# Optimization experiments

Measured on AMD Instinct MI355X. Metric: run time of the kernel, lower is better.

## Reference

```python
import jax, jax.numpy as jnp
import numpy as np

B, N, C, H = 8, 4096, 512, 8
HD = C // H  # head_dim = 64
SCALE = HD ** -0.5


def setup_inputs() -> dict:
    key = jax.random.key(0)
    k1, k2, k3, k4 = jax.random.split(key, 4)
    x1 = jax.random.normal(k1, (B, N, C), dtype=jnp.float32)
    x2 = jax.random.normal(k2, (B, N, C), dtype=jnp.float32)
    # nn.Linear(dim, 2*dim, bias=False) weights; stored as [in, out] for x @ W
    lim = 1.0 / np.sqrt(C)
    W_kv1 = jax.random.uniform(k3, (C, 2 * C), dtype=jnp.float32, minval=-lim, maxval=lim)
    W_kv2 = jax.random.uniform(k4, (C, 2 * C), dtype=jnp.float32, minval=-lim, maxval=lim)
    return {"x1": x1, "x2": x2, "W_kv1": W_kv1, "W_kv2": W_kv2}


def _heads(t):
    # [B, N, C] -> [B, H, N, HD]
    return t.reshape(B, N, H, HD).transpose(0, 2, 1, 3)


def _kv(x, W):
    kv = (x @ W).reshape(B, N, 2, H, HD)  # [B, N, 2, H, HD]
    kv = kv.transpose(2, 0, 3, 1, 4)      # [2, B, H, N, HD]
    return kv[0], kv[1]


def _ctx(k, v):
    # K^T V: [B, H, HD, HD], scaled then softmax over axis -2 (the k-feature axis)
    ctx = jnp.einsum("bhnd,bhne->bhde", k, v) * SCALE
    return jax.nn.softmax(ctx, axis=-2)


def reference(x1, x2, W_kv1, W_kv2):
    q1 = _heads(x1)
    q2 = _heads(x2)
    k1, v1 = _kv(x1, W_kv1)
    k2, v2 = _kv(x2, W_kv2)
    ctx1 = _ctx(k1, v1)
    ctx2 = _ctx(k2, v2)
    # cross: q1 attends via ctx2, q2 via ctx1
    o1 = jnp.einsum("bhnd,bhde->bhne", q1, ctx2).transpose(0, 2, 1, 3).reshape(B, N, C)
    o2 = jnp.einsum("bhnd,bhde->bhne", q2, ctx1).transpose(0, 2, 1, 3).reshape(B, N, C)
    return o1, o2
```

## Files before the change

kernel.cpp:

```cpp
#include <hip/hip_runtime.h>
#include <stdint.h>
#include <stddef.h>

#define NB 8
#define NSEQ 4096
#define NC 512
#define NH 8
#define SWZ(c) ((((c) >> 2) ^ (c)) & 7)

typedef __attribute__((ext_vector_type(4))) float f4;
typedef __attribute__((ext_vector_type(8))) short bf8;
typedef __attribute__((ext_vector_type(4))) short bf4;
typedef __attribute__((ext_vector_type(2))) unsigned int u32x2;
typedef __attribute__((ext_vector_type(4))) unsigned int u32x4;

__device__ __forceinline__ short f2bf(float f) {
  union { float f; unsigned int u; } v; v.f = f;
  unsigned int u = v.u + 0x7FFFu + ((v.u >> 16) & 1u);
  return (short)(u >> 16);
}
__device__ __forceinline__ float bf2f(short h) {
  union { unsigned int u; float f; } v;
  v.u = ((unsigned int)(unsigned short)h) << 16;
  return v.f;
}
__device__ __forceinline__ unsigned int cvtpk(float a, float b) {
  unsigned int r;
  asm("v_cvt_pk_bf16_f32 %0, %1, %2" : "=v"(r) : "v"(a), "v"(b));
  return r;
}

__global__ __launch_bounds__(256) void k_wt(const float* __restrict__ W0,
                                            const float* __restrict__ W1,
                                            short* __restrict__ Wth,
                                            short* __restrict__ Wtl) {
  __shared__ float t[64 * 65];
  int bid = blockIdx.x;
  int ot = bid & 15;
  int ct = (bid >> 4) & 7;
  int s = bid >> 7;
  const float* W = s ? W1 : W0;
  const float* src = W + (size_t)(ct * 64) * 1024 + ot * 64;
  int tid = threadIdx.x;
  int rr = tid >> 4, c4 = (tid & 15) * 4;
#pragma unroll
  for (int p = 0; p < 4; ++p) {
    int c = p * 16 + rr;
    f4 v = *(const f4*)&src[(size_t)c * 1024 + c4];
#pragma unroll
    for (int i = 0; i < 4; ++i) t[(c4 + i) * 65 + c] = v[i];
  }
  __syncthreads();
  size_t obase = (size_t)s * 524288 + (size_t)(ot * 64) * 512 + ct * 64;
#pragma unroll
  for (int p = 0; p < 4; ++p) {
    int o = p * 16 + rr;
    bf4 vh, vl;
#pragma unroll
    for (int i = 0; i < 4; ++i) {
      float v = t[o * 65 + c4 + i];
      short h = f2bf(v);
      vh[i] = h; vl[i] = f2bf(v - bf2f(h));
    }
    *(bf4*)&Wth[obase + (size_t)o * 512 + c4] = vh;
    *(bf4*)&Wtl[obase + (size_t)o * 512 + c4] = vl;
  }
}

__global__ __launch_bounds__(256) void k_xbt(const float* __restrict__ x0,
                                             const float* __restrict__ x1,
                                             short* __restrict__ XbT) {
  __shared__ short t[64 * 64];
  int bx = blockIdx.x;
  int ct = bx & 7;
  int nt = (bx >> 3) & 63;
  int b  = (bx >> 9) & 7;
  int s  = bx >> 12;
  const float* x = s ? x1 : x0;
  const float* xb = x + ((size_t)b * NSEQ + (size_t)nt * 64) * NC + ct * 64;
  int tid = threadIdx.x;
  int c4 = (tid & 15) * 4;
  int nb = (tid >> 4) * 4;
  int g = nb >> 3;
  int nlo = nb & 7;
  f4 v[4];
#pragma unroll
  for (int i = 0; i < 4; ++i)
    v[i] = *(const f4*)&xb[(size_t)(nb + i) * NC + c4];
#pragma unroll
  for (int ci = 0; ci < 4; ++ci) {
    int c = c4 + ci;
    int soff = c * 64 + ((g ^ SWZ(c)) << 3) + nlo;
    u32x2 wa;
    wa[0] = cvtpk(v[0][ci], v[1][ci]);
    wa[1] = cvtpk(v[2][ci], v[3][ci]);
    *(u32x2*)&t[soff] = wa;
  }
  __syncthreads();
  int gg = tid & 7;
  int cr = tid >> 3;
  short* Xp = XbT + ((size_t)(s * 8 + b) * NC + (size_t)ct * 64) * NSEQ + (size_t)nt * 64;
#pragma unroll
  for (int p = 0; p < 2; ++p) {
    int c = cr + p * 32;
    bf8 vv = *(const bf8*)&t[c * 64 + ((gg ^ SWZ(c)) << 3)];
    *(bf8*)&Xp[(size_t)c * NSEQ + gg * 8] = vv;
  }
}

__global__ __launch_bounds__(256) void k_gram(const short* __restrict__ XbT,
                                              float* __restrict__ G32) {
  __shared__ short Ab[3][64 * 64];
  __shared__ short Bb[3][64 * 64];
  int bid = blockIdx.x;
  int xcd = bid & 7;
  int j = bid >> 3;
  int sb = xcd + ((j >= 36) ? 8 : 0);
  int p = (j >= 36) ? (j - 36) : j;
  int ti = 0;
  while (p >= 8 - ti) { p -= 8 - ti; ++ti; }
  int tj = ti + p;
  int diag = (ti == tj);
  const short* Ar = XbT + ((size_t)sb * NC + ti * 64) * NSEQ;
  const short* Br = XbT + ((size_t)sb * NC + tj * 64) * NSEQ;
  int tid = threadIdx.x;
  int lane = tid & 63;
  int w = tid >> 6;
  int lrow = lane >> 3;
  int lgr = lane & 7;
  int wr = w & 1, wc = w >> 1;
  int mrow = lane & 15;
  int kreg = lane >> 4;
  f4 z = {0.f, 0.f, 0.f, 0.f};
  f4 acc[2][2];
#pragma unroll
  for (int i = 0; i < 2; ++i)
#pragma unroll
    for (int jq = 0; jq < 2; ++jq) acc[i][jq] = z;

  auto stage = [&](int t) {
    int buf = t % 3;
    int k0 = t * 64;
#pragma unroll
    for (int q = 0; q < 2; ++q) {
      int r0 = q * 32 + w * 8;
      int arow = r0 + lrow;
      int gsw = (lgr ^ lrow) << 3;
      __builtin_amdgcn_global_load_lds(
          (const unsigned int*)(Ar + (size_t)arow * NSEQ + k0 + gsw),
          (unsigned int*)&Ab[buf][r0 * 64], 16, 0, 0);
      if (!diag)
        __builtin_amdgcn_global_load_lds(
            (const unsigned int*)(Br + (size_t)arow * NSEQ + k0 + gsw),
            (unsigned int*)&Bb[buf][r0 * 64], 16, 0, 0);
    }
  };
  auto comp = [&](int buf) {
    const short* Abuf = Ab[buf];
    const short* Bbuf = diag ? Ab[buf] : Bb[buf];
#pragma unroll
    for (int kk = 0; kk < 2; ++kk) {
      int gr = kk * 4 + kreg;
      bf8 a[2], bb[2];
#pragma unroll
      for (int i = 0; i < 2; ++i) {
        int ra = wr * 32 + i * 16 + mrow;
        a[i] = *(const bf8*)&Abuf[ra * 64 + ((gr ^ (ra & 7)) << 3)];
        int rb2 = wc * 32 + i * 16 + mrow;
        bb[i] = *(const bf8*)&Bbuf[rb2 * 64 + ((gr ^ (rb2 & 7)) << 3)];
      }
#pragma unroll
      for (int i = 0; i < 2; ++i)
#pragma unroll
        for (int jq = 0; jq < 2; ++jq)
          acc[i][jq] = __builtin_amdgcn_mfma_f32_16x16x32_bf16(a[i], bb[jq], acc[i][jq], 0, 0, 0);
    }
  };

  stage(0);
  stage(1);
  for (int t = 0; t < 64; ++t) {
    if (t < 63) {
      if (diag) { asm volatile("s_waitcnt vmcnt(2)" ::: "memory"); }
      else      { asm volatile("s_waitcnt vmcnt(4)" ::: "memory"); }
    } else {
      asm volatile("s_waitcnt vmcnt(0)" ::: "memory");
    }
    __builtin_amdgcn_sched_barrier(0);
    __builtin_amdgcn_s_barrier();
    __builtin_amdgcn_sched_barrier(0);
    if (t + 2 < 64) stage(t + 2);
    __builtin_amdgcn_sched_barrier(0);
    comp(t % 3);
  }

  float* Gp = G32 + (size_t)sb * NC * NC;
  int rb = ti * 64 + wr * 32 + (lane >> 4) * 4;
  int cb = tj * 64 + wc * 32 + (lane & 15);
#pragma unroll
  for (int i = 0; i < 2; ++i)
#pragma unroll
    for (int jq = 0; jq < 2; ++jq)
#pragma unroll
      for (int r = 0; r < 4; ++r)
        Gp[(size_t)(rb + i * 16 + r) * NC + cb + jq * 16] = acc[i][jq][r];
}

__global__ __launch_bounds__(256) void k_sym(const float* __restrict__ G32,
                                             short* __restrict__ Gh,
                                             short* __restrict__ Gl) {
  __shared__ float t[64 * 65];
  int bid = blockIdx.x;
  int tile = bid & 63;
  int sb = bid >> 6;
  int ti = tile >> 3, tj = tile & 7;
  int tr = ti > tj;
  const float* src = G32 + (size_t)sb * 262144
                   + (tr ? ((size_t)(tj * 64) * 512 + ti * 64)
                         : ((size_t)(ti * 64) * 512 + tj * 64));
  int tid = threadIdx.x;
  int rr = tid >> 4;
  int c4 = (tid & 15) * 4;
#pragma unroll
  for (int p = 0; p < 4; ++p) {
    int r = p * 16 + rr;
    f4 v = *(const f4*)&src[(size_t)r * 512 + c4];
    if (tr) {
#pragma unroll
      for (int i = 0; i < 4; ++i) t[(c4 + i) * 65 + r] = v[i];
    } else {
#pragma unroll
      for (int i = 0; i < 4; ++i) t[r * 65 + c4 + i] = v[i];
    }
  }
  __syncthreads();
  size_t obase = (size_t)sb * 262144 + (size_t)(ti * 64) * 512 + tj * 64;
#pragma unroll
  for (int p = 0; p < 4; ++p) {
    int r = p * 16 + rr;
    bf4 vh, vl;
#pragma unroll
    for (int i = 0; i < 4; ++i) {
      float v = t[r * 65 + c4 + i] * 0.125f;
      short h = f2bf(v);
      vh[i] = h; vl[i] = f2bf(v - bf2f(h));
    }
    *(bf4*)&Gh[obase + (size_t)r * 512 + c4] = vh;
    *(bf4*)&Gl[obase + (size_t)r * 512 + c4] = vl;
  }
}

__global__ __launch_bounds__(256) void k_t(const short* __restrict__ Wth,
                                           const short* __restrict__ Wtl,
                                           const short* __restrict__ Gh,
                                           const short* __restrict__ Gl,
                                           float* __restrict__ Ttf) {
  __shared__ short Ah[128 * 40];
  __shared__ short Al[128 * 40];
  __shared__ short Bh[128 * 40];
  __shared__ short Bl[128 * 40];
  int tid = threadIdx.x;
  int et = blockIdx.x & 3;
  int ct = blockIdx.x >> 2;
  int sb = blockIdx.y;
  int s = sb >> 3;
  const short* Avh = Wth + ((size_t)s * 1024 + 512 + (size_t)et * 128) * NC;
  const short* Avl = Wtl + ((size_t)s * 1024 + 512 + (size_t)et * 128) * NC;
  const short* Gph = Gh + (size_t)sb * 262144 + (size_t)(ct * 128) * 512;
  const short* Gpl = Gl + (size_t)sb * 262144 + (size_t)(ct * 128) * 512;
  int cc = tid >> 1;
  int kh = (tid & 1) * 16;
  int lane = tid & 63;
  int w = tid >> 6;
  int wm = (w & 1) * 64;
  int wn = (w >> 1) * 64;
  int mrow = lane & 15;
  int kcol = (lane >> 4) * 8;
  f4 z = {0.f, 0.f, 0.f, 0.f};
  f4 acc[4][4];
#pragma unroll
  for (int i = 0; i < 4; ++i)
#pragma unroll
    for (int j = 0; j < 4; ++j) acc[i][j] = z;

  for (int it = 0; it < 16; ++it) {
    int k0 = it * 32;
    __syncthreads();
    *(bf8*)&Ah[cc * 40 + kh]     = *(const bf8*)&Avh[(size_t)cc * NC + k0 + kh];
    *(bf8*)&Ah[cc * 40 + kh + 8] = *(const bf8*)&Avh[(size_t)cc * NC + k0 + kh + 8];
    *(bf8*)&Al[cc * 40 + kh]     = *(const bf8*)&Avl[(size_t)cc * NC + k0 + kh];
    *(bf8*)&Al[cc * 40 + kh + 8] = *(const bf8*)&Avl[(size_t)cc * NC + k0 + kh + 8];
    *(bf8*)&Bh[cc * 40 + kh]     = *(const bf8*)&Gph[(size_t)cc * 512 + k0 + kh];
    *(bf8*)&Bh[cc * 40 + kh + 8] = *(const bf8*)&Gph[(size_t)cc * 512 + k0 + kh + 8];
    *(bf8*)&Bl[cc * 40 + kh]     = *(const bf8*)&Gpl[(size_t)cc * 512 + k0 + kh];
    *(bf8*)&Bl[cc * 40 + kh + 8] = *(const bf8*)&Gpl[(size_t)cc * 512 + k0 + kh + 8];
    __syncthreads();
    bf8 ah[4], al[4], bh[4], bl[4];
#pragma unroll
    for (int i = 0; i < 4; ++i) {
      ah[i] = *(const bf8*)&Ah[(wm + i * 16 + mrow) * 40 + kcol];
      al[i] = *(const bf8*)&Al[(wm + i * 16 + mrow) * 40 + kcol];
      bh[i] = *(const bf8*)&Bh[(wn + i * 16 + mrow) * 40 + kcol];
      bl[i] = *(const bf8*)&Bl[(wn + i * 16 + mrow) * 40 + kcol];
    }
#pragma unroll
    for (int i = 0; i < 4; ++i)
#pragma unroll
      for (int j = 0; j < 4; ++j) {
        acc[i][j] = __builtin_amdgcn_mfma_f32_16x16x32_bf16(ah[i], bh[j], acc[i][j], 0, 0, 0);
        acc[i][j] = __builtin_amdgcn_mfma_f32_16x16x32_bf16(ah[i], bl[j], acc[i][j], 0, 0, 0);
        acc[i][j] = __builtin_amdgcn_mfma_f32_16x16x32_bf16(al[i], bh[j], acc[i][j], 0, 0, 0);
      }
  }
  float* Tp = Ttf + (size_t)sb * NC * NC;
  int rb = et * 128 + wm + (lane >> 4) * 4;
  int cb = ct * 128 + wn + (lane & 15);
#pragma unroll
  for (int i = 0; i < 4; ++i)
#pragma unroll
    for (int j = 0; j < 4; ++j)
#pragma unroll
      for (int r = 0; r < 4; ++r)
        Tp[(size_t)(rb + i * 16 + r) * NC + cb + j * 16] = acc[i][j][r];
}

__global__ __launch_bounds__(256) void k_ctx(const short* __restrict__ Wth,
                                             const short* __restrict__ Wtl,
                                             const float* __restrict__ Ttf,
                                             short* __restrict__ ctxT) {
  __shared__ short Ah[64 * 72];
  __shared__ short Al[64 * 72];
  __shared__ short Bh[64 * 72];
  __shared__ short Bl[64 * 72];
  __shared__ float Sf[64 * 68];
  int tid = threadIdx.x;
  int h = blockIdx.x & 7;
  int sb = blockIdx.x >> 3;
  int s = sb >> 3;
  const short* Akh = Wth + ((size_t)s * 1024 + (size_t)h * 64) * NC;
  const short* Akl = Wtl + ((size_t)s * 1024 + (size_t)h * 64) * NC;
  const float* Bt = Ttf + ((size_t)sb * NC + (size_t)h * 64) * NC;
  int cs = tid >> 3;
  int kg = (tid & 7) * 8;
  int lane = tid & 63;
  int w = tid >> 6;
  int mrow = lane & 15;
  int kcol = (lane >> 4) * 8;
  f4 z = {0.f, 0.f, 0.f, 0.f};
  f4 acc[4];
#pragma unroll
  for (int j = 0; j < 4; ++j) acc[j] = z;

  for (int it = 0; it < 8; ++it) {
    int k0 = it * 64;
    __syncthreads();
#pragma unroll
    for (int r = 0; r < 2; ++r) {
      int d = cs + r * 32;
      *(bf8*)&Ah[d * 72 + kg] = *(const bf8*)&Akh[(size_t)d * NC + k0 + kg];
      *(bf8*)&Al[d * 72 + kg] = *(const bf8*)&Akl[(size_t)d * NC + k0 + kg];
      f4 g0 = *(const f4*)&Bt[(size_t)d * NC + k0 + kg];
      f4 g1 = *(const f4*)&Bt[(size_t)d * NC + k0 + kg + 4];
      bf8 vh, vl;
#pragma unroll
      for (int i = 0; i < 4; ++i) {
        short hh = f2bf(g0[i]);
        vh[i] = hh; vl[i] = f2bf(g0[i] - bf2f(hh));
        hh = f2bf(g1[i]);
        vh[i + 4] = hh; vl[i + 4] = f2bf(g1[i] - bf2f(hh));
      }
      *(bf8*)&Bh[d * 72 + kg] = vh;
      *(bf8*)&Bl[d * 72 + kg] = vl;
    }
    __syncthreads();
#pragma unroll
    for (int kk = 0; kk < 2; ++kk) {
      bf8 ah = *(const bf8*)&Ah[(w * 16 + mrow) * 72 + kk * 32 + kcol];
      bf8 al = *(const bf8*)&Al[(w * 16 + mrow) * 72 + kk * 32 + kcol];
#pragma unroll
      for (int j = 0; j < 4; ++j) {
        bf8 bh = *(const bf8*)&Bh[(j * 16 + mrow) * 72 + kk * 32 + kcol];
        bf8 bl = *(const bf8*)&Bl[(j * 16 + mrow) * 72 + kk * 32 + kcol];
        acc[j] = __builtin_amdgcn_mfma_f32_16x16x32_bf16(ah, bh, acc[j], 0, 0, 0);
        acc[j] = __builtin_amdgcn_mfma_f32_16x16x32_bf16(ah, bl, acc[j], 0, 0, 0);
        acc[j] = __builtin_amdgcn_mfma_f32_16x16x32_bf16(al, bh, acc[j], 0, 0, 0);
      }
    }
  }
  __syncthreads();
#pragma unroll
  for (int j = 0; j < 4; ++j)
#pragma unroll
    for (int r = 0; r < 4; ++r)
      Sf[(w * 16 + (lane >> 4) * 4 + r) * 68 + j * 16 + (lane & 15)] = acc[j][r];
  __syncthreads();
  if (tid < 64) {
    int e = tid;
    float mx = -1e30f;
    for (int d = 0; d < 64; ++d) mx = fmaxf(mx, Sf[d * 68 + e]);
    float sum = 0.f;
    for (int d = 0; d < 64; ++d) {
      float ev = __expf(Sf[d * 68 + e] - mx);
      sum += ev;
      Sf[d * 68 + e] = ev;
    }
    float rs = 1.f / sum;
    short* cp = ctxT + (((size_t)sb * NH + h) * 64 + e) * 64;
    for (int d0 = 0; d0 < 64; d0 += 4) {
      bf4 ov;
      ov[0] = f2bf(Sf[(d0 + 0) * 68 + e] * rs);
      ov[1] = f2bf(Sf[(d0 + 1) * 68 + e] * rs);
      ov[2] = f2bf(Sf[(d0 + 2) * 68 + e] * rs);
      ov[3] = f2bf(Sf[(d0 + 3) * 68 + e] * rs);
      *(bf4*)&cp[d0] = ov;
    }
  }
}

__global__ __launch_bounds__(256) void k_o(const float* __restrict__ x0,
                                           const float* __restrict__ x1,
                                           const short* __restrict__ ctxT,
                                           float* __restrict__ out) {
  __shared__ short Ab[128 * 72];
  __shared__ short Bb[64 * 72];
  int tid = threadIdx.x;
  int bx = blockIdx.x;
  int nt = bx & 31;
  int h = (bx >> 5) & 7;
  int b = (bx >> 8) & 7;
  int so = bx >> 11;
  const float* x = so ? x1 : x0;
  const short* cp = ctxT + (((size_t)(1 - so) * NB + b) * NH + h) * 64 * 64;
  {
    int e = tid >> 2;
    int dg = (tid & 3) * 16;
    *(bf8*)&Bb[e * 72 + dg] = *(const bf8*)&cp[e * 64 + dg];
    *(bf8*)&Bb[e * 72 + dg + 8] = *(const bf8*)&cp[e * 64 + dg + 8];
  }
  const float* xp = x + ((size_t)b * NSEQ + (size_t)nt * 128) * NC + h * 64;
  {
    int n = tid >> 1;
    int dh = (tid & 1) * 32;
    const float* row = xp + (size_t)n * NC + dh;
#pragma unroll
    for (int q = 0; q < 4; ++q) {
      f4 v0 = *(const f4*)&row[q * 8];
      f4 v1 = *(const f4*)&row[q * 8 + 4];
      u32x4 pw;
      pw[0] = cvtpk(v0[0], v0[1]);
      pw[1] = cvtpk(v0[2], v0[3]);
      pw[2] = cvtpk(v1[0], v1[1]);
      pw[3] = cvtpk(v1[2], v1[3]);
      *(u32x4*)&Ab[n * 72 + dh + q * 8] = pw;
    }
  }
  __syncthreads();
  int lane = tid & 63;
  int w = tid >> 6;
  int mrow = lane & 15;
  int kcol = (lane >> 4) * 8;
  f4 z = {0.f, 0.f, 0.f, 0.f};
  f4 acc[2][4];
#pragma unroll
  for (int i = 0; i < 2; ++i)
#pragma unroll
    for (int j = 0; j < 4; ++j) acc[i][j] = z;
#pragma unroll
  for (int kk = 0; kk < 2; ++kk) {
    bf8 a0 = *(const bf8*)&Ab[(w * 32 + mrow) * 72 + kk * 32 + kcol];
    bf8 a1 = *(const bf8*)&Ab[(w * 32 + 16 + mrow) * 72 + kk * 32 + kcol];
#pragma unroll
    for (int j = 0; j < 4; ++j) {
      bf8 bv = *(const bf8*)&Bb[(j * 16 + mrow) * 72 + kk * 32 + kcol];
      acc[0][j] = __builtin_amdgcn_mfma_f32_16x16x32_bf16(a0, bv, acc[0][j], 0, 0, 0);
      acc[1][j] = __builtin_amdgcn_mfma_f32_16x16x32_bf16(a1, bv, acc[1][j], 0, 0, 0);
    }
  }
  float* op = out + (size_t)so * ((size_t)NB * NSEQ * NC)
            + ((size_t)b * NSEQ + (size_t)nt * 128) * NC + h * 64;
#pragma unroll
  for (int i = 0; i < 2; ++i)
#pragma unroll
    for (int j = 0; j < 4; ++j)
#pragma unroll
      for (int r = 0; r < 4; ++r)
        op[(size_t)(w * 32 + i * 16 + (lane >> 4) * 4 + r) * NC + j * 16 + (lane & 15)] = acc[i][j][r];
}

extern "C" void kernel_launch(void* const* d_in, const int* in_sizes, int n_in,
                              void* d_out, int out_size, void* d_ws, size_t ws_size,
                              hipStream_t stream) {
  const float* x1 = (const float*)d_in[0];
  const float* x2 = (const float*)d_in[1];
  const float* W1 = (const float*)d_in[2];
  const float* W2 = (const float*)d_in[3];
  float* out = (float*)d_out;
  char* ws = (char*)d_ws;
  short* XbT  = (short*)ws;
  float* Ttf  = (float*)ws;
  short* Gh   = (short*)(ws + 16777216);
  short* Gl   = (short*)(ws + 25165824);
  short* Wth  = (short*)(ws + 67108864);
  short* Wtl  = (short*)(ws + 69206016);
  float* G32  = (float*)(ws + 71303168);
  short* ctxT = (short*)(ws + 88080384);

  hipLaunchKernelGGL(k_wt,   dim3(256),    dim3(256), 0, stream, W1, W2, Wth, Wtl);
  hipLaunchKernelGGL(k_xbt,  dim3(8192),   dim3(256), 0, stream, x1, x2, XbT);
  hipLaunchKernelGGL(k_gram, dim3(576),    dim3(256), 0, stream, XbT, G32);
  hipLaunchKernelGGL(k_sym,  dim3(1024),   dim3(256), 0, stream, G32, Gh, Gl);
  hipLaunchKernelGGL(k_t,    dim3(16, 16), dim3(256), 0, stream, Wth, Wtl, Gh, Gl, Ttf);
  hipLaunchKernelGGL(k_ctx,  dim3(128),    dim3(256), 0, stream, Wth, Wtl, Ttf, ctxT);
  hipLaunchKernelGGL(k_o,    dim3(4096),   dim3(256), 0, stream, x1, x2, ctxT, out);
}
```

Measured before the change: 184.2 us.

## Split off-diagonal Gram tiles along K, sum halves in k_sym, stage k_o output

The Gram kernel now uses 1024 blocks instead of 576. Off-diagonal tiles are split into two K halves: one half writes to the upper triangle, the other to the transposed lower slot. This balances work, since diagonal tiles run 64 iterations and each off-diagonal half runs 32. k_sym sums the upper and lower partials for off-diagonal tiles. The pipeline drops from triple buffering with manual vmcnt waits to double buffering with __syncthreads, which may expose more load latency. k_o now stages its output through LDS so rows are written to global memory with contiguous f4 stores.

```diff
diff --git a/kernel.cpp b/kernel.cpp
--- a/kernel.cpp
+++ b/kernel.cpp
@@ -110,19 +110,23 @@
 
 __global__ __launch_bounds__(256) void k_gram(const short* __restrict__ XbT,
                                               float* __restrict__ G32) {
-  __shared__ short Ab[3][64 * 64];
-  __shared__ short Bb[3][64 * 64];
+  __shared__ short Ab[2][64 * 64];
+  __shared__ short Bb[2][64 * 64];
   int bid = blockIdx.x;
-  int xcd = bid & 7;
-  int j = bid >> 3;
-  int sb = xcd + ((j >= 36) ? 8 : 0);
-  int p = (j >= 36) ? (j - 36) : j;
+  int L = (bid & 7) * 128 + (bid >> 3);
+  int sb = L >> 6;
+  int v = L & 63;
+  int half = (v >= 36);
+  int p = half ? v - 36 : v;
   int ti = 0;
-  while (p >= 8 - ti) { p -= 8 - ti; ++ti; }
-  int tj = ti + p;
-  int diag = (ti == tj);
-  const short* Ar = XbT + ((size_t)sb * NC + ti * 64) * NSEQ;
-  const short* Br = XbT + ((size_t)sb * NC + tj * 64) * NSEQ;
+  if (!half) { while (p >= 8 - ti) { p -= 8 - ti; ++ti; } }
+  else       { while (p >= 7 - ti) { p -= 7 - ti; ++ti; } }
+  int tj = half ? (ti + 1 + p) : (ti + p);
+  int diag = (!half) && (ti == tj);
+  int NIT = diag ? 64 : 32;
+  int kbase = half ? 2048 : 0;
+  const short* Ar = XbT + ((size_t)sb * NC + ti * 64) * NSEQ + kbase;
+  const short* Br = XbT + ((size_t)sb * NC + tj * 64) * NSEQ + kbase;
   int tid = threadIdx.x;
   int lane = tid & 63;
   int w = tid >> 6;
@@ -138,9 +142,7 @@
 #pragma unroll
     for (int jq = 0; jq < 2; ++jq) acc[i][jq] = z;
 
-  auto stage = [&](int t) {
-    int buf = t % 3;
-    int k0 = t * 64;
+  auto stage = [&](int buf, int k0) {
 #pragma unroll
     for (int q = 0; q < 2; ++q) {
       int r0 = q * 32 + w * 8;
@@ -177,26 +179,18 @@
     }
   };
 
-  stage(0);
-  stage(1);
-  for (int t = 0; t < 64; ++t) {
-    if (t < 63) {
-      if (diag) { asm volatile("s_waitcnt vmcnt(2)" ::: "memory"); }
-      else      { asm volatile("s_waitcnt vmcnt(4)" ::: "memory"); }
-    } else {
-      asm volatile("s_waitcnt vmcnt(0)" ::: "memory");
-    }
-    __builtin_amdgcn_sched_barrier(0);
-    __builtin_amdgcn_s_barrier();
-    __builtin_amdgcn_sched_barrier(0);
-    if (t + 2 < 64) stage(t + 2);
-    __builtin_amdgcn_sched_barrier(0);
-    comp(t % 3);
+  stage(0, 0);
+  for (int t = 0; t < NIT; ++t) {
+    __syncthreads();
+    if (t + 1 < NIT) stage((t + 1) & 1, (t + 1) * 64);
+    comp(t & 1);
   }
 
   float* Gp = G32 + (size_t)sb * NC * NC;
-  int rb = ti * 64 + wr * 32 + (lane >> 4) * 4;
-  int cb = tj * 64 + wc * 32 + (lane & 15);
+  int rpart = wr * 32 + (lane >> 4) * 4;
+  int cpart = wc * 32 + (lane & 15);
+  int rb = (half ? tj : ti) * 64 + rpart;
+  int cb = (half ? ti : tj) * 64 + cpart;
 #pragma unroll
   for (int i = 0; i < 2; ++i)
 #pragma unroll
@@ -215,22 +209,27 @@
   int sb = bid >> 6;
   int ti = tile >> 3, tj = tile & 7;
   int tr = ti > tj;
-  const float* src = G32 + (size_t)sb * 262144
-                   + (tr ? ((size_t)(tj * 64) * 512 + ti * 64)
-                         : ((size_t)(ti * 64) * 512 + tj * 64));
+  int umin = tr ? tj : ti, umax = tr ? ti : tj;
+  int offd = (umin != umax);
+  const float* srcU = G32 + (size_t)sb * 262144 + (size_t)(umin * 64) * 512 + umax * 64;
+  const float* srcL = G32 + (size_t)sb * 262144 + (size_t)(umax * 64) * 512 + umin * 64;
   int tid = threadIdx.x;
   int rr = tid >> 4;
   int c4 = (tid & 15) * 4;
 #pragma unroll
   for (int p = 0; p < 4; ++p) {
     int r = p * 16 + rr;
-    f4 v = *(const f4*)&src[(size_t)r * 512 + c4];
+    f4 vv = *(const f4*)&srcU[(size_t)r * 512 + c4];
+    if (offd) {
+      f4 v2 = *(const f4*)&srcL[(size_t)r * 512 + c4];
+      vv += v2;
+    }
     if (tr) {
 #pragma unroll
-      for (int i = 0; i < 4; ++i) t[(c4 + i) * 65 + r] = v[i];
+      for (int i = 0; i < 4; ++i) t[(c4 + i) * 65 + r] = vv[i];
     } else {
 #pragma unroll
-      for (int i = 0; i < 4; ++i) t[r * 65 + c4 + i] = v[i];
+      for (int i = 0; i < 4; ++i) t[r * 65 + c4 + i] = vv[i];
     }
   }
   __syncthreads();
@@ -421,8 +420,10 @@
                                            const float* __restrict__ x1,
                                            const short* __restrict__ ctxT,
                                            float* __restrict__ out) {
-  __shared__ short Ab[128 * 72];
-  __shared__ short Bb[64 * 72];
+  __shared__ float U[8704];
+  short* Ab = (short*)U;
+  short* Bb = (short*)U + 128 * 72;
+  float* OutT = U;
   int tid = threadIdx.x;
   int bx = blockIdx.x;
   int nt = bx & 31;
@@ -476,15 +477,22 @@
       acc[1][j] = __builtin_amdgcn_mfma_f32_16x16x32_bf16(a1, bv, acc[1][j], 0, 0, 0);
     }
   }
-  float* op = out + (size_t)so * ((size_t)NB * NSEQ * NC)
-            + ((size_t)b * NSEQ + (size_t)nt * 128) * NC + h * 64;
+  __syncthreads();
 #pragma unroll
   for (int i = 0; i < 2; ++i)
 #pragma unroll
     for (int j = 0; j < 4; ++j)
 #pragma unroll
       for (int r = 0; r < 4; ++r)
-        op[(size_t)(w * 32 + i * 16 + (lane >> 4) * 4 + r) * NC + j * 16 + (lane & 15)] = acc[i][j][r];
+        OutT[(w * 32 + i * 16 + (lane >> 4) * 4 + r) * 68 + j * 16 + (lane & 15)] = acc[i][j][r];
+  __syncthreads();
+  int r2 = tid >> 1;
+  int ch = (tid & 1) * 32;
+  float* op2 = out + (size_t)so * ((size_t)NB * NSEQ * NC)
+             + ((size_t)b * NSEQ + (size_t)nt * 128 + r2) * NC + h * 64 + ch;
+#pragma unroll
+  for (int q = 0; q < 8; ++q)
+    *(f4*)&op2[q * 4] = *(const f4*)&OutT[r2 * 68 + ch + q * 4];
 }
 
 extern "C" void kernel_launch(void* const* d_in, const int* in_sizes, int n_in,
@@ -507,7 +515,7 @@
 
   hipLaunchKernelGGL(k_wt,   dim3(256),    dim3(256), 0, stream, W1, W2, Wth, Wtl);
   hipLaunchKernelGGL(k_xbt,  dim3(8192),   dim3(256), 0, stream, x1, x2, XbT);
-  hipLaunchKernelGGL(k_gram, dim3(576),    dim3(256), 0, stream, XbT, G32);
+  hipLaunchKernelGGL(k_gram, dim3(1024),   dim3(256), 0, stream, XbT, G32);
   hipLaunchKernelGGL(k_sym,  dim3(1024),   dim3(256), 0, stream, G32, Gh, Gl);
   hipLaunchKernelGGL(k_t,    dim3(16, 16), dim3(256), 0, stream, Wth, Wtl, Gh, Gl, Ttf);
   hipLaunchKernelGGL(k_ctx,  dim3(128),    dim3(256), 0, stream, Wth, Wtl, Ttf, ctxT);
```

Result: slower. 189.2 us (+2.7%).
